# Performance work log

Measured on AMD Instinct MI355X. Metric: run time of the kernel, lower is better.

## Reference

```python
import jax, jax.numpy as jnp
import numpy as np

RADIUS = 11.0  # init kwarg
N, D = 8192, 64


def setup_inputs() -> dict:
    key = jax.random.key(0)
    kx, ka = jax.random.split(key)
    x = jax.random.normal(kx, (N, D), dtype=jnp.float32)
    adj = jax.random.randint(ka, (N, 16), 0, N, dtype=jnp.int32)  # unused by the layer
    return {"x": x, "adj": adj}


def reference(x, adj):
    # Pairwise Euclidean distances via Gram trick (same math as
    # sqrt(sum((x_i - x_j)^2)) but avoids materializing the [N, N, D] diff).
    sq = jnp.sum(x * x, axis=-1)                       # [N]
    d2 = sq[:, None] + sq[None, :] - 2.0 * (x @ x.T)    # [N, N]
    distances = jnp.sqrt(jnp.maximum(d2, 0.0))          # [N, N]
    mask = (distances <= RADIUS).astype(x.dtype)        # binary ball-query mask
    attention_scores = jax.nn.softmax(mask, axis=-1)    # softmax over 0/1 scores
    return attention_scores @ x                          # [N, D]
```

## Files before the change

kernel.cpp:

```cpp
#include <hip/hip_runtime.h>
#include <hip/hip_bf16.h>


#define NROWS 8192
#define DDIM  64

typedef __bf16 bf16x8 __attribute__((ext_vector_type(8)));
typedef float  f32x4  __attribute__((ext_vector_type(4)));

#define MFMA16(A, B, C) __builtin_amdgcn_mfma_f32_16x16x32_bf16((A), (B), (C), 0, 0, 0)

static __device__ __forceinline__ unsigned short bf16rn(float f) {
    unsigned u = __float_as_uint(f);
    unsigned r = u + 0x7FFFu + ((u >> 16) & 1u);
    return (unsigned short)(r >> 16);
}
static __device__ __forceinline__ float bf16tof(unsigned short h) {
    return __uint_as_float(((unsigned)h) << 16);
}

__global__ __launch_bounds__(256) void prep_hilo(const float* __restrict__ x,
                                                 unsigned short* __restrict__ xhi,
                                                 unsigned short* __restrict__ xlo,
                                                 float* __restrict__ sq) {
    int t = blockIdx.x * 256 + threadIdx.x;
    int row = t >> 4, q = t & 15;
    const float4 v = *(const float4*)(x + ((size_t)row << 6) + (q << 2));
    float f0 = v.x, f1 = v.y, f2 = v.z, f3 = v.w;
    unsigned short h0 = bf16rn(f0), h1 = bf16rn(f1), h2 = bf16rn(f2), h3 = bf16rn(f3);
    unsigned short l0 = bf16rn(f0 - bf16tof(h0));
    unsigned short l1 = bf16rn(f1 - bf16tof(h1));
    unsigned short l2 = bf16rn(f2 - bf16tof(h2));
    unsigned short l3 = bf16rn(f3 - bf16tof(h3));
    float ss = f0 * f0;
    ss = fmaf(f1, f1, ss); ss = fmaf(f2, f2, ss); ss = fmaf(f3, f3, ss);
    uint2 ph, pl;
    ph.x = (unsigned)h0 | ((unsigned)h1 << 16);
    ph.y = (unsigned)h2 | ((unsigned)h3 << 16);
    pl.x = (unsigned)l0 | ((unsigned)l1 << 16);
    pl.y = (unsigned)l2 | ((unsigned)l3 << 16);
    *(uint2*)(xhi + ((size_t)row << 6) + (q << 2)) = ph;
    *(uint2*)(xlo + ((size_t)row << 6) + (q << 2)) = pl;
    ss += __shfl_xor(ss, 1);
    ss += __shfl_xor(ss, 2);
    ss += __shfl_xor(ss, 4);
    ss += __shfl_xor(ss, 8);
    if (q == 0) sq[row] = ss;
}

__global__ __launch_bounds__(256) void prep_coltot(const float* __restrict__ x,
                                                   float* __restrict__ stot) {
    __shared__ float red[4][64];
    int g = blockIdx.x;
    int col = threadIdx.x & 63, rg = threadIdx.x >> 6;
    float s = 0.f;
    int base = g * 128 + rg;
    for (int k = 0; k < 32; ++k)
        s += x[(size_t)(base + 4 * k) * 64 + col];
    red[rg][col] = s;
    __syncthreads();
    if (threadIdx.x < 64) {
        float v = red[0][threadIdx.x] + red[1][threadIdx.x] +
                  red[2][threadIdx.x] + red[3][threadIdx.x];
        atomicAdd(stot + threadIdx.x, v);
    }
}

__global__ __launch_bounds__(256, 2) void ballq_main(
        const unsigned short* __restrict__ xhi,
        const unsigned short* __restrict__ xlo,
        const float* __restrict__ sq,
        float* __restrict__ Spart, float* __restrict__ cpart, int nchunk) {
    __shared__ unsigned short sJhi[64][72];
    __shared__ unsigned short sJlo[64][72];
    __shared__ unsigned short sJT [64][72];
    __shared__ unsigned short sM  [128][72];
    __shared__ float sqJ[64];
    __shared__ float cred[128];

    const int tid = threadIdx.x;
    const int w = tid >> 6, l = tid & 63;
    const int l16 = l & 15, lg = l >> 4;
    const int wi = w >> 1, wj = w & 1;
    const int itile = blockIdx.x & 63, chunk = blockIdx.x >> 6;
    const int i0 = itile << 7;

    if (tid < 128) cred[tid] = 0.f;

    bf16x8 ahi[4][2], alo[4][2];
    float sqi[4][4];
#pragma unroll
    for (int mt = 0; mt < 4; ++mt) {
        int ib = i0 + wi * 64 + mt * 16;
#pragma unroll
        for (int ks = 0; ks < 2; ++ks) {
            size_t off = (size_t)(ib + l16) * 64 + ks * 32 + lg * 8;
            ahi[mt][ks] = *(const bf16x8*)(xhi + off);
            alo[mt][ks] = *(const bf16x8*)(xlo + off);
        }
#pragma unroll
        for (int r = 0; r < 4; ++r) sqi[mt][r] = sq[ib + lg * 4 + r];
    }

    f32x4 accS[4][2];
    float cacc[4][4];
#pragma unroll
    for (int a = 0; a < 4; ++a)
#pragma unroll
        for (int b = 0; b < 2; ++b) {
            accS[a][b][0] = 0.f; accS[a][b][1] = 0.f;
            accS[a][b][2] = 0.f; accS[a][b][3] = 0.f;
        }
#pragma unroll
    for (int a = 0; a < 4; ++a)
#pragma unroll
        for (int r = 0; r < 4; ++r) cacc[a][r] = 0.f;

    const int sj  = (tid & 31) * 2;
    const int sd0 = (tid >> 5) * 8;

    const int jpt = 128 / nchunk;
    const int jt0 = chunk * jpt;

    for (int jt = jt0; jt < jt0 + jpt; ++jt) {
        const int j0 = jt << 6;
        uint4 h0 = *(const uint4*)(xhi + (size_t)(j0 + sj) * 64 + sd0);
        uint4 h1 = *(const uint4*)(xhi + (size_t)(j0 + sj + 1) * 64 + sd0);
        uint4 q0 = *(const uint4*)(xlo + (size_t)(j0 + sj) * 64 + sd0);
        uint4 q1 = *(const uint4*)(xlo + (size_t)(j0 + sj + 1) * 64 + sd0);
        *(uint4*)&sJhi[sj][sd0]     = h0;
        *(uint4*)&sJhi[sj + 1][sd0] = h1;
        *(uint4*)&sJlo[sj][sd0]     = q0;
        *(uint4*)&sJlo[sj + 1][sd0] = q1;
        const unsigned short* a0 = (const unsigned short*)&h0;
        const unsigned short* a1 = (const unsigned short*)&h1;
#pragma unroll
        for (int e = 0; e < 8; ++e) {
            unsigned pv = (unsigned)a0[e] | ((unsigned)a1[e] << 16);
            *(unsigned*)&sJT[sd0 + e][sj] = pv;
        }
        if (tid < 64) sqJ[tid] = sq[j0 + tid];
        __syncthreads();

        bf16x8 bhi[2][2], blo[2][2];
#pragma unroll
        for (int nt = 0; nt < 2; ++nt)
#pragma unroll
            for (int ks = 0; ks < 2; ++ks) {
                int jr = wj * 32 + nt * 16 + l16;
                bhi[nt][ks] = *(const bf16x8*)&sJhi[jr][ks * 32 + lg * 8];
                blo[nt][ks] = *(const bf16x8*)&sJlo[jr][ks * 32 + lg * 8];
            }
        f32x4 accD[4][2];
#pragma unroll
        for (int a = 0; a < 4; ++a)
#pragma unroll
            for (int b = 0; b < 2; ++b) {
                accD[a][b][0] = 0.f; accD[a][b][1] = 0.f;
                accD[a][b][2] = 0.f; accD[a][b][3] = 0.f;
            }
#pragma unroll
        for (int mt = 0; mt < 4; ++mt)
#pragma unroll
            for (int nt = 0; nt < 2; ++nt)
#pragma unroll
                for (int ks = 0; ks < 2; ++ks) {
                    accD[mt][nt] = MFMA16(ahi[mt][ks], bhi[nt][ks], accD[mt][nt]);
                    accD[mt][nt] = MFMA16(ahi[mt][ks], blo[nt][ks], accD[mt][nt]);
                    accD[mt][nt] = MFMA16(alo[mt][ks], bhi[nt][ks], accD[mt][nt]);
                }

        float sqjv0 = sqJ[wj * 32 + l16];
        float sqjv1 = sqJ[wj * 32 + 16 + l16];
#pragma unroll
        for (int mt = 0; mt < 4; ++mt)
#pragma unroll
            for (int nt = 0; nt < 2; ++nt) {
                float sqj = nt ? sqjv1 : sqjv0;
#pragma unroll
                for (int r = 0; r < 4; ++r) {
                    float d2 = fmaf(accD[mt][nt][r], -2.0f, sqi[mt][r] + sqj);
                    bool in = (d2 <= 121.0f);
                    cacc[mt][r] += in ? 1.0f : 0.0f;
                    sM[wi * 64 + mt * 16 + lg * 4 + r][wj * 32 + nt * 16 + l16] =
                        in ? (unsigned short)0x3F80 : (unsigned short)0;
                }
            }
        __syncthreads();

        bf16x8 am[4][2], bT[2][2];
#pragma unroll
        for (int mt = 0; mt < 4; ++mt)
#pragma unroll
            for (int ks = 0; ks < 2; ++ks)
                am[mt][ks] = *(const bf16x8*)&sM[wi * 64 + mt * 16 + l16][ks * 32 + lg * 8];
#pragma unroll
        for (int nt = 0; nt < 2; ++nt)
#pragma unroll
            for (int ks = 0; ks < 2; ++ks)
                bT[nt][ks] = *(const bf16x8*)&sJT[wj * 32 + nt * 16 + l16][ks * 32 + lg * 8];
#pragma unroll
        for (int mt = 0; mt < 4; ++mt)
#pragma unroll
            for (int nt = 0; nt < 2; ++nt)
#pragma unroll
                for (int ks = 0; ks < 2; ++ks)
                    accS[mt][nt] = MFMA16(am[mt][ks], bT[nt][ks], accS[mt][nt]);
        __syncthreads();
    }

#pragma unroll
    for (int mt = 0; mt < 4; ++mt)
#pragma unroll
        for (int r = 0; r < 4; ++r) {
            float v = cacc[mt][r];
            v += __shfl_xor(v, 1);
            v += __shfl_xor(v, 2);
            v += __shfl_xor(v, 4);
            v += __shfl_xor(v, 8);
            if (l16 == 0) atomicAdd(&cred[wi * 64 + mt * 16 + lg * 4 + r], v);
        }
    __syncthreads();
    if (tid < 128) cpart[(size_t)chunk * NROWS + i0 + tid] = cred[tid];

#pragma unroll
    for (int mt = 0; mt < 4; ++mt)
#pragma unroll
        for (int nt = 0; nt < 2; ++nt)
#pragma unroll
            for (int r = 0; r < 4; ++r) {
                size_t row = (size_t)chunk * NROWS + i0 + wi * 64 + mt * 16 + lg * 4 + r;
                Spart[row * 64 + wj * 32 + nt * 16 + l16] = accS[mt][nt][r];
            }
}

__global__ __launch_bounds__(256) void ballq_combine(
        const float* __restrict__ Spart, const float* __restrict__ cpart,
        const float* __restrict__ stot, float* __restrict__ out, int nchunk) {
    int t = blockIdx.x * 256 + threadIdx.x;
    int i = t >> 6, d = t & 63;
    float s = 0.f, c = 0.f;
    for (int ch = 0; ch < nchunk; ++ch) {
        s += Spart[((size_t)ch * NROWS + i) * 64 + d];
        c += cpart[(size_t)ch * NROWS + i];
    }
    const float K = 0.36787944117144233f;
    float num = s + K * (stot[d] - s);
    float den = c + K * (8192.0f - c);
    out[t] = num / den;
}

extern "C" void kernel_launch(void* const* d_in, const int* in_sizes, int n_in,
                              void* d_out, int out_size, void* d_ws, size_t ws_size,
                              hipStream_t stream) {
    (void)in_sizes; (void)n_in; (void)out_size;
    const float* x = (const float*)d_in[0];
    float* out = (float*)d_out;
    char* ws = (char*)d_ws;

    unsigned short* xhi = (unsigned short*)ws;
    unsigned short* xlo = (unsigned short*)(ws + (1u << 20));
    float* sq   = (float*)(ws + (2u << 20));
    float* stot = (float*)(ws + (2u << 20) + 32768);
    size_t fixed = (2u << 20) + 32768 + 256;
    char* dyn = ws + fixed;

    int nchunk = 8;
    while (nchunk > 1 &&
           fixed + (size_t)nchunk * NROWS * 4 + (size_t)nchunk * NROWS * 64 * 4 > ws_size)
        nchunk >>= 1;
    float* cpart = (float*)dyn;
    float* Spart = (float*)(dyn + (size_t)nchunk * NROWS * 4);

    hipMemsetAsync(stot, 0, 256, stream);
    prep_hilo<<<512, 256, 0, stream>>>(x, xhi, xlo, sq);
    prep_coltot<<<64, 256, 0, stream>>>(x, stot);
    ballq_main<<<64 * nchunk, 256, 0, stream>>>(xhi, xlo, sq, Spart, cpart, nchunk);
    ballq_combine<<<2048, 256, 0, stream>>>(Spart, cpart, stot, out, nchunk);
}
```

Baseline: 122.7 us.

## Restructure ball-query kernel: register-resident mask, double-buffered J tiles, atomic reduction

```diff
diff --git a/kernel.cpp b/kernel.cpp
--- a/kernel.cpp
+++ b/kernel.cpp
@@ -7,6 +7,8 @@
 
 typedef __bf16 bf16x8 __attribute__((ext_vector_type(8)));
 typedef float  f32x4  __attribute__((ext_vector_type(4)));
+typedef unsigned int u32;
+typedef u32 u32x4 __attribute__((ext_vector_type(4)));
 
 #define MFMA16(A, B, C) __builtin_amdgcn_mfma_f32_16x16x32_bf16((A), (B), (C), 0, 0, 0)
 
@@ -19,10 +21,12 @@
     return __uint_as_float(((unsigned)h) << 16);
 }
 
-__global__ __launch_bounds__(256) void prep_hilo(const float* __restrict__ x,
-                                                 unsigned short* __restrict__ xhi,
-                                                 unsigned short* __restrict__ xlo,
-                                                 float* __restrict__ sq) {
+__global__ __launch_bounds__(256) void prep(const float* __restrict__ x,
+                                            unsigned short* __restrict__ xhi,
+                                            unsigned short* __restrict__ xlo,
+                                            float* __restrict__ sq,
+                                            float* __restrict__ stot) {
+    __shared__ float sp[4][64];
     int t = blockIdx.x * 256 + threadIdx.x;
     int row = t >> 4, q = t & 15;
     const float4 v = *(const float4*)(x + ((size_t)row << 6) + (q << 2));
@@ -32,125 +36,111 @@
     unsigned short l1 = bf16rn(f1 - bf16tof(h1));
     unsigned short l2 = bf16rn(f2 - bf16tof(h2));
     unsigned short l3 = bf16rn(f3 - bf16tof(h3));
+    uint2 ph, pl;
+    ph.x = (u32)h0 | ((u32)h1 << 16);  ph.y = (u32)h2 | ((u32)h3 << 16);
+    pl.x = (u32)l0 | ((u32)l1 << 16);  pl.y = (u32)l2 | ((u32)l3 << 16);
+    *(uint2*)(xhi + ((size_t)row << 6) + (q << 2)) = ph;
+    *(uint2*)(xlo + ((size_t)row << 6) + (q << 2)) = pl;
     float ss = f0 * f0;
     ss = fmaf(f1, f1, ss); ss = fmaf(f2, f2, ss); ss = fmaf(f3, f3, ss);
-    uint2 ph, pl;
-    ph.x = (unsigned)h0 | ((unsigned)h1 << 16);
-    ph.y = (unsigned)h2 | ((unsigned)h3 << 16);
-    pl.x = (unsigned)l0 | ((unsigned)l1 << 16);
-    pl.y = (unsigned)l2 | ((unsigned)l3 << 16);
-    *(uint2*)(xhi + ((size_t)row << 6) + (q << 2)) = ph;
-    *(uint2*)(xlo + ((size_t)row << 6) + (q << 2)) = pl;
-    ss += __shfl_xor(ss, 1);
-    ss += __shfl_xor(ss, 2);
-    ss += __shfl_xor(ss, 4);
-    ss += __shfl_xor(ss, 8);
+    ss += __shfl_xor(ss, 1); ss += __shfl_xor(ss, 2);
+    ss += __shfl_xor(ss, 4); ss += __shfl_xor(ss, 8);
     if (q == 0) sq[row] = ss;
-}
-
-__global__ __launch_bounds__(256) void prep_coltot(const float* __restrict__ x,
-                                                   float* __restrict__ stot) {
-    __shared__ float red[4][64];
-    int g = blockIdx.x;
-    int col = threadIdx.x & 63, rg = threadIdx.x >> 6;
-    float s = 0.f;
-    int base = g * 128 + rg;
-    for (int k = 0; k < 32; ++k)
-        s += x[(size_t)(base + 4 * k) * 64 + col];
-    red[rg][col] = s;
+    f0 += __shfl_xor(f0, 16); f0 += __shfl_xor(f0, 32);
+    f1 += __shfl_xor(f1, 16); f1 += __shfl_xor(f1, 32);
+    f2 += __shfl_xor(f2, 16); f2 += __shfl_xor(f2, 32);
+    f3 += __shfl_xor(f3, 16); f3 += __shfl_xor(f3, 32);
+    int l = threadIdx.x & 63, wv = threadIdx.x >> 6;
+    if (l < 16) {
+        sp[wv][l * 4 + 0] = f0; sp[wv][l * 4 + 1] = f1;
+        sp[wv][l * 4 + 2] = f2; sp[wv][l * 4 + 3] = f3;
+    }
     __syncthreads();
     if (threadIdx.x < 64) {
-        float v = red[0][threadIdx.x] + red[1][threadIdx.x] +
-                  red[2][threadIdx.x] + red[3][threadIdx.x];
-        atomicAdd(stot + threadIdx.x, v);
-    }
-}
-
-__global__ __launch_bounds__(256, 2) void ballq_main(
+        float s = sp[0][threadIdx.x] + sp[1][threadIdx.x] +
+                  sp[2][threadIdx.x] + sp[3][threadIdx.x];
+        atomicAdd(stot + threadIdx.x, s);
+    }
+}
+
+static __device__ __forceinline__ int jslot(int j) {
+    return (j & 32) | (((j >> 2) & 3) << 3) | (((j >> 4) & 1) << 2) | (j & 3);
+}
+static __device__ __forceinline__ char* jt_addr(char* base, int d, int bytecol) {
+    return base + d * 160 + (bytecol ^ ((d & 7) << 4));
+}
+
+__global__ __launch_bounds__(256, 3) void ballq_main(
         const unsigned short* __restrict__ xhi,
         const unsigned short* __restrict__ xlo,
         const float* __restrict__ sq,
-        float* __restrict__ Spart, float* __restrict__ cpart, int nchunk) {
-    __shared__ unsigned short sJhi[64][72];
-    __shared__ unsigned short sJlo[64][72];
-    __shared__ unsigned short sJT [64][72];
-    __shared__ unsigned short sM  [128][72];
-    __shared__ float sqJ[64];
-    __shared__ float cred[128];
+        float* __restrict__ S, float* __restrict__ cnt) {
+    __shared__ char sJT[2][64 * 160];
+    __shared__ float sqJ[2][64];
 
     const int tid = threadIdx.x;
-    const int w = tid >> 6, l = tid & 63;
-    const int l16 = l & 15, lg = l >> 4;
-    const int wi = w >> 1, wj = w & 1;
+    const int w = tid >> 6, l = tid & 63, l16 = l & 15, lg = l >> 4;
     const int itile = blockIdx.x & 63, chunk = blockIdx.x >> 6;
-    const int i0 = itile << 7;
-
-    if (tid < 128) cred[tid] = 0.f;
-
-    bf16x8 ahi[4][2], alo[4][2];
-    float sqi[4][4];
-#pragma unroll
-    for (int mt = 0; mt < 4; ++mt) {
-        int ib = i0 + wi * 64 + mt * 16;
+    const int i0 = (itile << 7) + w * 32;
+    const int jt0 = chunk * 10 + (chunk < 8 ? chunk : 8);
+    const int jtn = (chunk < 8) ? 11 : 10;
+
+    bf16x8 ihi[2][2], ilo[2][2];
+    float sqi[2];
+#pragma unroll
+    for (int mt = 0; mt < 2; ++mt) {
+        int ir = i0 + mt * 16 + l16;
 #pragma unroll
         for (int ks = 0; ks < 2; ++ks) {
-            size_t off = (size_t)(ib + l16) * 64 + ks * 32 + lg * 8;
-            ahi[mt][ks] = *(const bf16x8*)(xhi + off);
-            alo[mt][ks] = *(const bf16x8*)(xlo + off);
-        }
-#pragma unroll
-        for (int r = 0; r < 4; ++r) sqi[mt][r] = sq[ib + lg * 4 + r];
-    }
-
-    f32x4 accS[4][2];
-    float cacc[4][4];
-#pragma unroll
-    for (int a = 0; a < 4; ++a)
-#pragma unroll
-        for (int b = 0; b < 2; ++b) {
+            size_t off = (size_t)ir * 64 + ks * 32 + lg * 8;
+            ihi[mt][ks] = *(const bf16x8*)(xhi + off);
+            ilo[mt][ks] = *(const bf16x8*)(xlo + off);
+        }
+        sqi[mt] = sq[ir];
+    }
+
+    f32x4 accS[2][4];
+    u32 pcnt[2] = {0u, 0u};
+#pragma unroll
+    for (int a = 0; a < 2; ++a)
+#pragma unroll
+        for (int b = 0; b < 4; ++b) {
             accS[a][b][0] = 0.f; accS[a][b][1] = 0.f;
             accS[a][b][2] = 0.f; accS[a][b][3] = 0.f;
         }
-#pragma unroll
-    for (int a = 0; a < 4; ++a)
-#pragma unroll
-        for (int r = 0; r < 4; ++r) cacc[a][r] = 0.f;
-
-    const int sj  = (tid & 31) * 2;
+
+    const int sj = (tid & 31) * 2;
     const int sd0 = (tid >> 5) * 8;
-
-    const int jpt = 128 / nchunk;
-    const int jt0 = chunk * jpt;
-
-    for (int jt = jt0; jt < jt0 + jpt; ++jt) {
-        const int j0 = jt << 6;
+    const int sslot = jslot(sj);
+
+    {
+        int j0 = jt0 << 6;
         uint4 h0 = *(const uint4*)(xhi + (size_t)(j0 + sj) * 64 + sd0);
         uint4 h1 = *(const uint4*)(xhi + (size_t)(j0 + sj + 1) * 64 + sd0);
-        uint4 q0 = *(const uint4*)(xlo + (size_t)(j0 + sj) * 64 + sd0);
-        uint4 q1 = *(const uint4*)(xlo + (size_t)(j0 + sj + 1) * 64 + sd0);
-        *(uint4*)&sJhi[sj][sd0]     = h0;
-        *(uint4*)&sJhi[sj + 1][sd0] = h1;
-        *(uint4*)&sJlo[sj][sd0]     = q0;
-        *(uint4*)&sJlo[sj + 1][sd0] = q1;
+        float sqv = (tid < 64) ? sq[j0 + tid] : 0.f;
         const unsigned short* a0 = (const unsigned short*)&h0;
         const unsigned short* a1 = (const unsigned short*)&h1;
 #pragma unroll
         for (int e = 0; e < 8; ++e) {
-            unsigned pv = (unsigned)a0[e] | ((unsigned)a1[e] << 16);
-            *(unsigned*)&sJT[sd0 + e][sj] = pv;
-        }
-        if (tid < 64) sqJ[tid] = sq[j0 + tid];
-        __syncthreads();
-
-        bf16x8 bhi[2][2], blo[2][2];
-#pragma unroll
-        for (int nt = 0; nt < 2; ++nt)
-#pragma unroll
-            for (int ks = 0; ks < 2; ++ks) {
-                int jr = wj * 32 + nt * 16 + l16;
-                bhi[nt][ks] = *(const bf16x8*)&sJhi[jr][ks * 32 + lg * 8];
-                blo[nt][ks] = *(const bf16x8*)&sJlo[jr][ks * 32 + lg * 8];
-            }
+            u32 pv = (u32)a0[e] | ((u32)a1[e] << 16);
+            *(u32*)jt_addr(sJT[0], sd0 + e, sslot * 2) = pv;
+        }
+        if (tid < 64) sqJ[0][tid] = sqv;
+    }
+    __syncthreads();
+
+    int buf = 0;
+    for (int t = 0; t < jtn; ++t) {
+        const int j0 = (jt0 + t) << 6;
+        const bool more = (t + 1 < jtn);
+        uint4 n0, n1; float nsq = 0.f;
+        if (more) {
+            int jn = j0 + 64;
+            n0 = *(const uint4*)(xhi + (size_t)(jn + sj) * 64 + sd0);
+            n1 = *(const uint4*)(xhi + (size_t)(jn + sj + 1) * 64 + sd0);
+            if (tid < 64) nsq = sq[jn + tid];
+        }
+
         f32x4 accD[4][2];
 #pragma unroll
         for (int a = 0; a < 4; ++a)
@@ -160,100 +150,121 @@
                 accD[a][b][2] = 0.f; accD[a][b][3] = 0.f;
             }
 #pragma unroll
-        for (int mt = 0; mt < 4; ++mt)
-#pragma unroll
-            for (int nt = 0; nt < 2; ++nt)
+        for (int nt = 0; nt < 4; ++nt) {
+            bf16x8 jh[2], jl[2];
+#pragma unroll
+            for (int ks = 0; ks < 2; ++ks) {
+                size_t off = (size_t)(j0 + nt * 16 + l16) * 64 + ks * 32 + lg * 8;
+                jh[ks] = *(const bf16x8*)(xhi + off);
+                jl[ks] = *(const bf16x8*)(xlo + off);
+            }
+#pragma unroll
+            for (int mt = 0; mt < 2; ++mt)
 #pragma unroll
                 for (int ks = 0; ks < 2; ++ks) {
-                    accD[mt][nt] = MFMA16(ahi[mt][ks], bhi[nt][ks], accD[mt][nt]);
-                    accD[mt][nt] = MFMA16(ahi[mt][ks], blo[nt][ks], accD[mt][nt]);
-                    accD[mt][nt] = MFMA16(alo[mt][ks], bhi[nt][ks], accD[mt][nt]);
+                    accD[nt][mt] = MFMA16(jh[ks], ihi[mt][ks], accD[nt][mt]);
+                    accD[nt][mt] = MFMA16(jh[ks], ilo[mt][ks], accD[nt][mt]);
+                    accD[nt][mt] = MFMA16(jl[ks], ihi[mt][ks], accD[nt][mt]);
                 }
-
-        float sqjv0 = sqJ[wj * 32 + l16];
-        float sqjv1 = sqJ[wj * 32 + 16 + l16];
-#pragma unroll
-        for (int mt = 0; mt < 4; ++mt)
-#pragma unroll
-            for (int nt = 0; nt < 2; ++nt) {
-                float sqj = nt ? sqjv1 : sqjv0;
-#pragma unroll
-                for (int r = 0; r < 4; ++r) {
-                    float d2 = fmaf(accD[mt][nt][r], -2.0f, sqi[mt][r] + sqj);
-                    bool in = (d2 <= 121.0f);
-                    cacc[mt][r] += in ? 1.0f : 0.0f;
-                    sM[wi * 64 + mt * 16 + lg * 4 + r][wj * 32 + nt * 16 + l16] =
-                        in ? (unsigned short)0x3F80 : (unsigned short)0;
-                }
-            }
+        }
+
+        u32 Fw[2][8];
+#pragma unroll
+        for (int nt = 0; nt < 4; ++nt) {
+            const int kj = nt >> 1, s = nt & 1;
+            float sqr0 = sqJ[buf][nt * 16 + lg * 4 + 0];
+            float sqr1 = sqJ[buf][nt * 16 + lg * 4 + 1];
+            float sqr2 = sqJ[buf][nt * 16 + lg * 4 + 2];
+            float sqr3 = sqJ[buf][nt * 16 + lg * 4 + 3];
+#pragma unroll
+            for (int mt = 0; mt < 2; ++mt) {
+                float base = sqi[mt];
+                bool in0 = fmaf(-2.f, accD[nt][mt][0], base + sqr0) <= 121.f;
+                bool in1 = fmaf(-2.f, accD[nt][mt][1], base + sqr1) <= 121.f;
+                bool in2 = fmaf(-2.f, accD[nt][mt][2], base + sqr2) <= 121.f;
+                bool in3 = fmaf(-2.f, accD[nt][mt][3], base + sqr3) <= 121.f;
+                Fw[mt][kj * 4 + s * 2 + 0] =
+                    (in0 ? 0x3F80u : 0u) | (in1 ? 0x3F800000u : 0u);
+                Fw[mt][kj * 4 + s * 2 + 1] =
+                    (in2 ? 0x3F80u : 0u) | (in3 ? 0x3F800000u : 0u);
+            }
+        }
+#pragma unroll
+        for (int mt = 0; mt < 2; ++mt)
+#pragma unroll
+            for (int wd = 0; wd < 8; ++wd)
+                pcnt[mt] += (u32)__builtin_popcount(Fw[mt][wd]);
+
+#pragma unroll
+        for (int kj = 0; kj < 2; ++kj) {
+            u32x4 fa0 = {Fw[0][kj * 4 + 0], Fw[0][kj * 4 + 1],
+                         Fw[0][kj * 4 + 2], Fw[0][kj * 4 + 3]};
+            u32x4 fa1 = {Fw[1][kj * 4 + 0], Fw[1][kj * 4 + 1],
+                         Fw[1][kj * 4 + 2], Fw[1][kj * 4 + 3]};
+            bf16x8 m0 = __builtin_bit_cast(bf16x8, fa0);
+            bf16x8 m1 = __builtin_bit_cast(bf16x8, fa1);
+#pragma unroll
+            for (int ntd = 0; ntd < 4; ++ntd) {
+                const bf16x8* bp = (const bf16x8*)__builtin_assume_aligned(
+                    jt_addr(sJT[buf], ntd * 16 + l16, kj * 64 + lg * 16), 16);
+                bf16x8 bT = *bp;
+                accS[0][ntd] = MFMA16(m0, bT, accS[0][ntd]);
+                accS[1][ntd] = MFMA16(m1, bT, accS[1][ntd]);
+            }
+        }
+
+        if (more) {
+            const unsigned short* a0 = (const unsigned short*)&n0;
+            const unsigned short* a1 = (const unsigned short*)&n1;
+#pragma unroll
+            for (int e = 0; e < 8; ++e) {
+                u32 pv = (u32)a0[e] | ((u32)a1[e] << 16);
+                *(u32*)jt_addr(sJT[buf ^ 1], sd0 + e, sslot * 2) = pv;
+            }
+            if (tid < 64) sqJ[buf ^ 1][tid] = nsq;
+        }
         __syncthreads();
-
-        bf16x8 am[4][2], bT[2][2];
-#pragma unroll
-        for (int mt = 0; mt < 4; ++mt)
-#pragma unroll
-            for (int ks = 0; ks < 2; ++ks)
-                am[mt][ks] = *(const bf16x8*)&sM[wi * 64 + mt * 16 + l16][ks * 32 + lg * 8];
-#pragma unroll
-        for (int nt = 0; nt < 2; ++nt)
-#pragma unroll
-            for (int ks = 0; ks < 2; ++ks)
-                bT[nt][ks] = *(const bf16x8*)&sJT[wj * 32 + nt * 16 + l16][ks * 32 + lg * 8];
-#pragma unroll
-        for (int mt = 0; mt < 4; ++mt)
-#pragma unroll
-            for (int nt = 0; nt < 2; ++nt)
-#pragma unroll
-                for (int ks = 0; ks < 2; ++ks)
-                    accS[mt][nt] = MFMA16(am[mt][ks], bT[nt][ks], accS[mt][nt]);
-        __syncthreads();
-    }
-
-#pragma unroll
-    for (int mt = 0; mt < 4; ++mt)
-#pragma unroll
-        for (int r = 0; r < 4; ++r) {
-            float v = cacc[mt][r];
-            v += __shfl_xor(v, 1);
-            v += __shfl_xor(v, 2);
-            v += __shfl_xor(v, 4);
-            v += __shfl_xor(v, 8);
-            if (l16 == 0) atomicAdd(&cred[wi * 64 + mt * 16 + lg * 4 + r], v);
-        }
-    __syncthreads();
-    if (tid < 128) cpart[(size_t)chunk * NROWS + i0 + tid] = cred[tid];
-
-#pragma unroll
-    for (int mt = 0; mt < 4; ++mt)
-#pragma unroll
-        for (int nt = 0; nt < 2; ++nt)
+        buf ^= 1;
+    }
+
+#pragma unroll
+    for (int mt = 0; mt < 2; ++mt) {
+        u32 v = pcnt[mt];
+        v += __shfl_xor(v, 16);
+        v += __shfl_xor(v, 32);
+        if (lg == 0) atomicAdd(cnt + i0 + mt * 16 + l16, (float)(v / 7u));
+    }
+#pragma unroll
+    for (int mt = 0; mt < 2; ++mt)
+#pragma unroll
+        for (int ntd = 0; ntd < 4; ++ntd)
 #pragma unroll
             for (int r = 0; r < 4; ++r) {
-                size_t row = (size_t)chunk * NROWS + i0 + wi * 64 + mt * 16 + lg * 4 + r;
-                Spart[row * 64 + wj * 32 + nt * 16 + l16] = accS[mt][nt][r];
+                size_t idx = (size_t)(i0 + mt * 16 + lg * 4 + r) * 64 + ntd * 16 + l16;
+                atomicAdd(S + idx, accS[mt][ntd][r]);
             }
 }
 
 __global__ __launch_bounds__(256) void ballq_combine(
-        const float* __restrict__ Spart, const float* __restrict__ cpart,
-        const float* __restrict__ stot, float* __restrict__ out, int nchunk) {
+        const float* __restrict__ S, const float* __restrict__ cnt,
+        const float* __restrict__ stot, float* __restrict__ out) {
     int t = blockIdx.x * 256 + threadIdx.x;
-    int i = t >> 6, d = t & 63;
-    float s = 0.f, c = 0.f;
-    for (int ch = 0; ch < nchunk; ++ch) {
-        s += Spart[((size_t)ch * NROWS + i) * 64 + d];
-        c += cpart[(size_t)ch * NROWS + i];
-    }
+    int i = t >> 4, d0 = (t & 15) << 2;
+    float c = cnt[i];
+    f32x4 s = *(const f32x4*)(S + (size_t)i * 64 + d0);
+    f32x4 st = *(const f32x4*)(stot + d0);
     const float K = 0.36787944117144233f;
-    float num = s + K * (stot[d] - s);
-    float den = c + K * (8192.0f - c);
-    out[t] = num / den;
+    float den = 1.f / (c + K * (8192.f - c));
+    f32x4 o;
+#pragma unroll
+    for (int k = 0; k < 4; ++k) o[k] = (s[k] + K * (st[k] - s[k])) * den;
+    *(f32x4*)(out + (size_t)i * 64 + d0) = o;
 }
 
 extern "C" void kernel_launch(void* const* d_in, const int* in_sizes, int n_in,
                               void* d_out, int out_size, void* d_ws, size_t ws_size,
                               hipStream_t stream) {
-    (void)in_sizes; (void)n_in; (void)out_size;
+    (void)in_sizes; (void)n_in; (void)out_size; (void)ws_size;
     const float* x = (const float*)d_in[0];
     float* out = (float*)d_out;
     char* ws = (char*)d_ws;
@@ -261,20 +272,12 @@
     unsigned short* xhi = (unsigned short*)ws;
     unsigned short* xlo = (unsigned short*)(ws + (1u << 20));
     float* sq   = (float*)(ws + (2u << 20));
-    float* stot = (float*)(ws + (2u << 20) + 32768);
-    size_t fixed = (2u << 20) + 32768 + 256;
-    char* dyn = ws + fixed;
-
-    int nchunk = 8;
-    while (nchunk > 1 &&
-           fixed + (size_t)nchunk * NROWS * 4 + (size_t)nchunk * NROWS * 64 * 4 > ws_size)
-        nchunk >>= 1;
-    float* cpart = (float*)dyn;
-    float* Spart = (float*)(dyn + (size_t)nchunk * NROWS * 4);
-
-    hipMemsetAsync(stot, 0, 256, stream);
-    prep_hilo<<<512, 256, 0, stream>>>(x, xhi, xlo, sq);
-    prep_coltot<<<64, 256, 0, stream>>>(x, stot);
-    ballq_main<<<64 * nchunk, 256, 0, stream>>>(xhi, xlo, sq, Spart, cpart, nchunk);
-    ballq_combine<<<2048, 256, 0, stream>>>(Spart, cpart, stot, out, nchunk);
-}
+    float* S    = (float*)(ws + (2u << 20) + 32768);
+    float* cnt  = (float*)(ws + (2u << 20) + 32768 + (1u << 21));
+    float* stot = (float*)(ws + (2u << 20) + 32768 + (1u << 21) + 32768);
+
+    hipMemsetAsync(S, 0, (1u << 21) + 32768 + 256, stream);
+    prep<<<512, 256, 0, stream>>>(x, xhi, xlo, sq, stot);
+    ballq_main<<<64 * 12, 256, 0, stream>>>(xhi, xlo, sq, S, cnt);
+    ballq_combine<<<512, 256, 0, stream>>>(S, cnt, stot, out);
+}
```

After: 156.4 us. 27.5% more time.
